# Performance work log

Measured on AMD Instinct MI355X. Metric: run time of the kernel, lower is better.

The kernel has to match this reference:

```python
import jax, jax.numpy as jnp
import numpy as np

N_ATOMS = 8192
MAX_NEIGHBORS = 12
MAX_RADIUS = 8.0
NUM_BINS = 50
WIDTH = 0.2


def setup_inputs() -> dict:
    key = jax.random.key(0)
    # uniform distances in [0,1): all within max_radius, so every node has
    # >= MAX_NEIGHBORS valid neighbors -> fixed output shape N*MAX_NEIGHBORS
    dm = jax.random.uniform(key, (N_ATOMS, N_ATOMS), dtype=jnp.float32)
    return {"distance_matrix": dm}


def reference(distance_matrix):
    n = distance_matrix.shape[0]
    # radius threshold: entries beyond max_radius are excluded from selection
    masked = jnp.where(distance_matrix <= MAX_RADius_const(), distance_matrix, jnp.inf) if False else jnp.where(distance_matrix <= MAX_RADIUS, distance_matrix, jnp.inf)
    # per-node smallest-k neighbors == original global-sort + per-node first-k
    _, nbr_idx = jax.lax.top_k(-masked, MAX_NEIGHBORS)  # [n, k]
    dists = jnp.take_along_axis(distance_matrix, nbr_idx, axis=1)  # [n, k]
    src = jnp.broadcast_to(jnp.arange(n, dtype=nbr_idx.dtype)[:, None], (n, MAX_NEIGHBORS))
    edge_index = jnp.stack([src, nbr_idx], axis=-1).reshape(-1, 2)  # [n*k, 2]
    # Gaussian RBF expansion
    centers = jnp.linspace(0.0, 1.0, NUM_BINS)  # [NUM_BINS]
    z = (dists[..., None] - centers) / WIDTH  # [n, k, NUM_BINS]
    edge_features = jnp.exp(-0.5 * z * z).reshape(-1, NUM_BINS)  # [n*k, NUM_BINS]
    return edge_index, edge_features
```

## Files before the change

### kernel.cpp

```cpp
#include <hip/hip_runtime.h>
#include <math.h>


#define N_ATOMS 8192
#define K 12
#define NBINS 50
#define CAP 1024
#define BLOCK 256
#define MAX_RADIUS 8.0f
#define CAND_T 0.01f

__global__ __launch_bounds__(BLOCK) void edge_kernel(const float* __restrict__ dm,
                                                     float* __restrict__ out) {
    const int row = blockIdx.x;
    const int tid = threadIdx.x;
    const float* rowp = dm + (size_t)row * N_ATOMS;
    const float4* row4 = (const float4*)rowp;

    __shared__ unsigned long long s_keys[CAP];
    __shared__ int s_count;
    __shared__ int s_selidx[K];
    __shared__ float s_seldist[K];
    __shared__ unsigned long long s_red[BLOCK];

    if (tid == 0) s_count = 0;
    __syncthreads();

    #pragma unroll
    for (int j = 0; j < N_ATOMS / (BLOCK * 4); ++j) {
        int v4 = tid + j * BLOCK;
        float4 v = row4[v4];
        int base = v4 * 4;
        float vals[4] = {v.x, v.y, v.z, v.w};
        #pragma unroll
        for (int c = 0; c < 4; ++c) {
            float d = vals[c];
            if (d < CAND_T) {
                int pos = atomicAdd(&s_count, 1);
                if (pos < CAP) {
                    unsigned long long fb = (unsigned long long)__float_as_uint(d);
                    s_keys[pos] = (fb << 32) | (unsigned int)(base + c);
                }
            }
        }
    }
    __syncthreads();
    int count = s_count;

    if (count >= K && count <= CAP) {
        for (int j = tid; j < count; j += BLOCK) {
            unsigned long long kj = s_keys[j];
            int rank = 0;
            for (int m = 0; m < count; ++m)
                rank += (s_keys[m] < kj) ? 1 : 0;
            if (rank < K) {
                s_selidx[rank] = (int)(kj & 0xFFFFFFFFull);
                s_seldist[rank] = __uint_as_float((unsigned int)(kj >> 32));
            }
        }
    } else {
        unsigned long long last = 0ULL;
        for (int r = 0; r < K; ++r) {
            unsigned long long best = ~0ULL;
            for (int j = 0; j < N_ATOMS / (BLOCK * 4); ++j) {
                int v4 = tid + j * BLOCK;
                float4 v = row4[v4];
                int base = v4 * 4;
                float vals[4] = {v.x, v.y, v.z, v.w};
                #pragma unroll
                for (int c = 0; c < 4; ++c) {
                    float d = vals[c];
                    float md = (d <= MAX_RADIUS) ? d : __uint_as_float(0x7F800000u);
                    unsigned long long key =
                        ((unsigned long long)__float_as_uint(md) << 32) |
                        (unsigned int)(base + c);
                    bool ok = (r == 0) || (key > last);
                    if (ok && key < best) best = key;
                }
            }
            s_red[tid] = best;
            __syncthreads();
            for (int s = BLOCK / 2; s > 0; s >>= 1) {
                if (tid < s) {
                    if (s_red[tid + s] < s_red[tid]) s_red[tid] = s_red[tid + s];
                }
                __syncthreads();
            }
            unsigned long long sel = s_red[0];
            if (tid == 0) {
                int idx = (int)(sel & 0xFFFFFFFFull);
                s_selidx[r] = idx;
                s_seldist[r] = rowp[idx];
            }
            last = sel;
            __syncthreads();
        }
    }
    __syncthreads();

    float* out_ei = out;
    float* out_ef = out + (size_t)N_ATOMS * K * 2;
    if (tid < 2 * K) {
        int r = tid >> 1, comp = tid & 1;
        out_ei[((size_t)row * K + r) * 2 + comp] =
            comp ? (float)s_selidx[r] : (float)row;
    }

    for (int t = tid; t < K * NBINS; t += BLOCK) {
        int r = t / NBINS, b = t - r * NBINS;
        float d = s_seldist[r];
        float c = (float)b / 49.0f;
        float z = (d - c) / 0.2f;
        out_ef[((size_t)row * K + r) * NBINS + b] = __expf(-0.5f * z * z);
    }
}

extern "C" void kernel_launch(void* const* d_in, const int* in_sizes, int n_in,
                              void* d_out, int out_size, void* d_ws, size_t ws_size,
                              hipStream_t stream) {
    const float* dm = (const float*)d_in[0];
    float* out = (float*)d_out;
    edge_kernel<<<N_ATOMS, BLOCK, 0, stream>>>(dm, out);
}
```

Measured before the change: 364.1 us.

## Process one row per wavefront with ballot compaction and shuffle reductions

Each 64-lane wavefront now owns one matrix row, with four rows per block, instead of one 256-thread block per row. Candidate collection uses wave ballot and popcount prefix compaction rather than shared-memory atomics. The fallback selection uses xor-shuffle reductions instead of block-wide shared-memory reductions with barriers. This removes atomics and most block synchronisation, but each lane now streams four times as much of the row, and the candidate capacity shrinks to 256 per row, which sends more rows to the slow fallback path if they exceed it.

```diff
diff --git a/kernel.cpp b/kernel.cpp
--- a/kernel.cpp
+++ b/kernel.cpp
@@ -5,113 +5,108 @@
 #define N_ATOMS 8192
 #define K 12
 #define NBINS 50
-#define CAP 1024
-#define BLOCK 256
+#define CAP 256
+#define WAVES 4
+#define BLOCK (WAVES * 64)
 #define MAX_RADIUS 8.0f
 #define CAND_T 0.01f
 
 __global__ __launch_bounds__(BLOCK) void edge_kernel(const float* __restrict__ dm,
                                                      float* __restrict__ out) {
-    const int row = blockIdx.x;
-    const int tid = threadIdx.x;
+    const int wave = threadIdx.x >> 6;
+    const int lane = threadIdx.x & 63;
+    const int row = blockIdx.x * WAVES + wave;
     const float* rowp = dm + (size_t)row * N_ATOMS;
     const float4* row4 = (const float4*)rowp;
 
-    __shared__ unsigned long long s_keys[CAP];
-    __shared__ int s_count;
-    __shared__ int s_selidx[K];
-    __shared__ float s_seldist[K];
-    __shared__ unsigned long long s_red[BLOCK];
+    __shared__ unsigned long long s_keys[WAVES][CAP];
+    __shared__ int s_selidx[WAVES][K];
+    __shared__ float s_seldist[WAVES][K];
 
-    if (tid == 0) s_count = 0;
-    __syncthreads();
+    const unsigned long long lane_below = (1ull << lane) - 1ull;
 
-    #pragma unroll
-    for (int j = 0; j < N_ATOMS / (BLOCK * 4); ++j) {
-        int v4 = tid + j * BLOCK;
+    int count = 0;
+    #pragma unroll 4
+    for (int i = 0; i < N_ATOMS / (64 * 4); ++i) {
+        int v4 = lane + i * 64;
         float4 v = row4[v4];
-        int base = v4 * 4;
+        int bidx = v4 * 4;
         float vals[4] = {v.x, v.y, v.z, v.w};
         #pragma unroll
         for (int c = 0; c < 4; ++c) {
             float d = vals[c];
-            if (d < CAND_T) {
-                int pos = atomicAdd(&s_count, 1);
-                if (pos < CAP) {
-                    unsigned long long fb = (unsigned long long)__float_as_uint(d);
-                    s_keys[pos] = (fb << 32) | (unsigned int)(base + c);
-                }
+            bool pred = d < CAND_T;
+            unsigned long long m = __ballot(pred);
+            if (pred) {
+                int pos = count + __popcll(m & lane_below);
+                if (pos < CAP)
+                    s_keys[wave][pos] =
+                        ((unsigned long long)__float_as_uint(d) << 32) |
+                        (unsigned int)(bidx + c);
             }
+            count += __popcll(m);
         }
     }
     __syncthreads();
-    int count = s_count;
 
     if (count >= K && count <= CAP) {
-        for (int j = tid; j < count; j += BLOCK) {
-            unsigned long long kj = s_keys[j];
+        for (int j = lane; j < count; j += 64) {
+            unsigned long long kj = s_keys[wave][j];
             int rank = 0;
-            for (int m = 0; m < count; ++m)
-                rank += (s_keys[m] < kj) ? 1 : 0;
+            for (int m2 = 0; m2 < count; ++m2)
+                rank += (s_keys[wave][m2] < kj) ? 1 : 0;
             if (rank < K) {
-                s_selidx[rank] = (int)(kj & 0xFFFFFFFFull);
-                s_seldist[rank] = __uint_as_float((unsigned int)(kj >> 32));
+                s_selidx[wave][rank] = (int)(kj & 0xFFFFFFFFull);
+                s_seldist[wave][rank] =
+                    __uint_as_float((unsigned int)(kj >> 32));
             }
         }
     } else {
-        unsigned long long last = 0ULL;
+        unsigned long long last = 0ull;
         for (int r = 0; r < K; ++r) {
-            unsigned long long best = ~0ULL;
-            for (int j = 0; j < N_ATOMS / (BLOCK * 4); ++j) {
-                int v4 = tid + j * BLOCK;
+            unsigned long long best = ~0ull;
+            for (int i = 0; i < N_ATOMS / (64 * 4); ++i) {
+                int v4 = lane + i * 64;
                 float4 v = row4[v4];
-                int base = v4 * 4;
+                int bidx = v4 * 4;
                 float vals[4] = {v.x, v.y, v.z, v.w};
                 #pragma unroll
                 for (int c = 0; c < 4; ++c) {
                     float d = vals[c];
-                    float md = (d <= MAX_RADIUS) ? d : __uint_as_float(0x7F800000u);
+                    float md = (d <= MAX_RADIUS) ? d
+                                                 : __uint_as_float(0x7F800000u);
                     unsigned long long key =
                         ((unsigned long long)__float_as_uint(md) << 32) |
-                        (unsigned int)(base + c);
-                    bool ok = (r == 0) || (key > last);
-                    if (ok && key < best) best = key;
+                        (unsigned int)(bidx + c);
+                    if (((r == 0) || (key > last)) && key < best) best = key;
                 }
             }
-            s_red[tid] = best;
-            __syncthreads();
-            for (int s = BLOCK / 2; s > 0; s >>= 1) {
-                if (tid < s) {
-                    if (s_red[tid + s] < s_red[tid]) s_red[tid] = s_red[tid + s];
-                }
-                __syncthreads();
+            #pragma unroll
+            for (int off = 32; off > 0; off >>= 1) {
+                unsigned long long other = __shfl_xor(best, off, 64);
+                if (other < best) best = other;
             }
-            unsigned long long sel = s_red[0];
-            if (tid == 0) {
-                int idx = (int)(sel & 0xFFFFFFFFull);
-                s_selidx[r] = idx;
-                s_seldist[r] = rowp[idx];
+            if (lane == 0) {
+                int idx = (int)(best & 0xFFFFFFFFull);
+                s_selidx[wave][r] = idx;
+                s_seldist[wave][r] = rowp[idx];
             }
-            last = sel;
-            __syncthreads();
+            last = best;
         }
     }
-    __syncthreads();
 
     float* out_ei = out;
     float* out_ef = out + (size_t)N_ATOMS * K * 2;
-    if (tid < 2 * K) {
-        int r = tid >> 1, comp = tid & 1;
+    if (lane < 2 * K) {
+        int r = lane >> 1, comp = lane & 1;
         out_ei[((size_t)row * K + r) * 2 + comp] =
-            comp ? (float)s_selidx[r] : (float)row;
+            comp ? (float)s_selidx[wave][r] : (float)row;
     }
-
-    for (int t = tid; t < K * NBINS; t += BLOCK) {
+    for (int t = lane; t < K * NBINS; t += 64) {
         int r = t / NBINS, b = t - r * NBINS;
-        float d = s_seldist[r];
-        float c = (float)b / 49.0f;
-        float z = (d - c) / 0.2f;
-        out_ef[((size_t)row * K + r) * NBINS + b] = __expf(-0.5f * z * z);
+        float d = s_seldist[wave][r];
+        float z = (d - (float)b * (1.0f / 49.0f)) * 5.0f;
+        out_ef[(size_t)row * K * NBINS + t] = __expf(-0.5f * z * z);
     }
 }
 
@@ -120,5 +115,5 @@
                               hipStream_t stream) {
     const float* dm = (const float*)d_in[0];
     float* out = (float*)d_out;
-    edge_kernel<<<N_ATOMS, BLOCK, 0, stream>>>(dm, out);
+    edge_kernel<<<N_ATOMS / WAVES, BLOCK, 0, stream>>>(dm, out);
 }
```

Result: no change. 366.1 us (+0.5%).
